# Kernel tuning notes

Measured on AMD Instinct MI355X. Metric: run time of the kernel, lower is better.

## Reference

```python
import jax, jax.numpy as jnp
import numpy as np


def setup_inputs() -> dict:
    key = jax.random.key(0)
    k1, k2, k3 = jax.random.split(key, 3)
    B, H, S, D = 1, 16, 2048, 64
    NPOS, HID = 64, 1024
    query = jax.random.normal(k1, (B, H, S, D), dtype=jnp.float32)
    attn_logits = jax.random.normal(k2, (B, H, S, S), dtype=jnp.float32)
    pos_emb = jax.random.normal(k3, (1, NPOS, HID), dtype=jnp.float32)
    return {"query": query, "attn_logits": attn_logits, "pos_emb": pos_emb}


def reference(query, attn_logits, pos_emb):
    # query: [B,H,S,D]; attn_logits: [B,H,S,S]; pos_emb: [1,NPOS,H*D]
    B, H, S, D = query.shape
    npos_max = pos_emb.shape[1]
    gates = jax.nn.sigmoid(attn_logits)
    # reverse cumsum along keys: position of each key relative to query
    pos = jnp.flip(jnp.cumsum(jnp.flip(gates, axis=-1), axis=-1), axis=-1)
    pos = jnp.minimum(pos, npos_max - 1)
    pos_ceil = jnp.ceil(pos).astype(jnp.int32)
    pos_floor = jnp.floor(pos).astype(jnp.int32)
    # split heads: [1,NPOS,H*D] -> [H,NPOS,D]
    pe = pos_emb.reshape(npos_max, H, D).transpose(1, 0, 2)
    # per-head position logits: [B,H,S,NPOS]
    logits_int = jnp.einsum('bhsd,hnd->bhsn', query, pe)
    logits_ceil = jnp.take_along_axis(logits_int, pos_ceil, axis=-1)
    logits_floor = jnp.take_along_axis(logits_int, pos_floor, axis=-1)
    w = pos - pos_floor  # fractional interpolation weight
    return logits_ceil * w + logits_floor * (1.0 - w)
```

## Files before the change

kernel.cpp:

```cpp
#include <hip/hip_runtime.h>

namespace {
constexpr int kH       = 16;
constexpr int kS       = 2048;
constexpr int kD       = 64;
constexpr int kNpos    = 64;
constexpr int kHid     = 1024;
constexpr int kChunk   = 256;
constexpr int kNChunks = kS / kChunk;
constexpr int kRowsPerBlock = 16;
}

__device__ __forceinline__ float dot4f(float4 a, float qx, float qy, float qz, float qw) {
    return fmaf(a.x, qx, fmaf(a.y, qy, fmaf(a.z, qz, a.w * qw)));
}

template <int CTRL, int ROWM>
__device__ __forceinline__ float dpp_add(float v) {
    int t = __builtin_amdgcn_update_dpp(0, __float_as_int(v), CTRL, ROWM, 0xf, true);
    return v + __int_as_float(t);
}

__device__ __forceinline__ float wave_incl_scan(float v) {
    v = dpp_add<0x111, 0xf>(v);
    v = dpp_add<0x112, 0xf>(v);
    v = dpp_add<0x114, 0xf>(v);
    v = dpp_add<0x118, 0xf>(v);
    v = dpp_add<0x142, 0xa>(v);
    v = dpp_add<0x143, 0xc>(v);
    return v;
}

__device__ __forceinline__ float bcast_lane(float v, int l) {
    return __int_as_float(__builtin_amdgcn_readlane(__float_as_int(v), l));
}

__device__ __forceinline__ void process_row(const float* __restrict__ arow,
                                            float* __restrict__ orow,
                                            float acc, float4 x0, int lane) {
    const float fill = bcast_lane(acc, kNpos - 1);
    float running = 0.0f;
    int c = kNChunks - 1;
    float4 x = x0;
    for (; c >= 0; --c) {
        if (c != kNChunks - 1)
            x = *reinterpret_cast<const float4*>(arow + c * kChunk + lane * 4);
        float g0 = 1.0f / (1.0f + __expf(-x.x));
        float g1 = 1.0f / (1.0f + __expf(-x.y));
        float g2 = 1.0f / (1.0f + __expf(-x.z));
        float g3 = 1.0f / (1.0f + __expf(-x.w));

        float e3 = g3;
        float e2 = e3 + g2;
        float e1 = e2 + g1;
        float e0 = e1 + g0;

        float incl  = wave_incl_scan(e0);
        float total = bcast_lane(incl, 63);
        float sfx   = running + (total - incl);

        float p[4] = {sfx + e0, sfx + e1, sfx + e2, sfx + e3};
        float r[4];
        #pragma unroll
        for (int i = 0; i < 4; ++i) {
            float pc = fminf(p[i], 63.0f);
            float fl = floorf(pc);
            float w  = pc - fl;
            int  fi  = (int)fl;
            int  ni  = (fi < kNpos - 1) ? fi + 1 : kNpos - 1;
            float lf = __shfl(acc, fi);
            float ln = __shfl(acc, ni);
            r[i] = fmaf(w, ln - lf, lf);
        }
        *reinterpret_cast<float4*>(orow + c * kChunk + lane * 4) =
            make_float4(r[0], r[1], r[2], r[3]);

        running += total;
        if (running >= 63.0f) break;
    }
    const int fillEnd = (c > 0) ? c * kChunk : 0;
    const float4 fv = make_float4(fill, fill, fill, fill);
    for (int j = lane * 4; j < fillEnd; j += 256) {
        *reinterpret_cast<float4*>(orow + j) = fv;
    }
}

__global__ __launch_bounds__(256) void cope_kernel(
    const float* __restrict__ query,
    const float* __restrict__ attn,
    const float* __restrict__ pos_emb,
    float* __restrict__ out)
{
    const int t    = threadIdx.x;
    const int lane = t & 63;
    const int wid  = t >> 6;
    const int row_base = blockIdx.x * kRowsPerBlock;
    const int h        = row_base >> 11;
    const int wrow = __builtin_amdgcn_readfirstlane(row_base + wid * 4);

    __shared__ float4 pe_lds[kNpos * 16];

    const float* arow = attn + (size_t)wrow * kS;
    float*       orow = out  + (size_t)wrow * kS;

    const int tail = (kNChunks - 1) * kChunk + lane * 4;
    float4 x0 = *reinterpret_cast<const float4*>(arow + 0 * kS + tail);
    float4 x1 = *reinterpret_cast<const float4*>(arow + 1 * kS + tail);
    float4 x2 = *reinterpret_cast<const float4*>(arow + 2 * kS + tail);
    float4 x3 = *reinterpret_cast<const float4*>(arow + 3 * kS + tail);

    #pragma unroll
    for (int k = 0; k < 4; ++k) {
        const int e = t + 256 * k;
        const int n = e >> 4;
        const int j = e & 15;
        float4 p = *reinterpret_cast<const float4*>(
            pos_emb + (size_t)n * kHid + h * kD + 4 * j);
        pe_lds[(n << 4) | (j ^ (n & 15))] = p;
    }
    __syncthreads();

    const float* qbase = query + (size_t)wrow * kD;
    float acc0 = 0.f, acc1 = 0.f, acc2 = 0.f, acc3 = 0.f;
    #pragma unroll 4
    for (int j = 0; j < 16; ++j) {
        float4 pe4 = pe_lds[(lane << 4) | (j ^ (lane & 15))];
        const float* q0 = qbase + 0 * kD + 4 * j;
        const float* q1 = qbase + 1 * kD + 4 * j;
        const float* q2 = qbase + 2 * kD + 4 * j;
        const float* q3 = qbase + 3 * kD + 4 * j;
        acc0 += dot4f(pe4, q0[0], q0[1], q0[2], q0[3]);
        acc1 += dot4f(pe4, q1[0], q1[1], q1[2], q1[3]);
        acc2 += dot4f(pe4, q2[0], q2[1], q2[2], q2[3]);
        acc3 += dot4f(pe4, q3[0], q3[1], q3[2], q3[3]);
    }

    process_row(arow + 0 * kS, orow + 0 * kS, acc0, x0, lane);
    process_row(arow + 1 * kS, orow + 1 * kS, acc1, x1, lane);
    process_row(arow + 2 * kS, orow + 2 * kS, acc2, x2, lane);
    process_row(arow + 3 * kS, orow + 3 * kS, acc3, x3, lane);
}

extern "C" void kernel_launch(void* const* d_in, const int* in_sizes, int n_in,
                              void* d_out, int out_size, void* d_ws, size_t ws_size,
                              hipStream_t stream) {
    const float* query   = (const float*)d_in[0];
    const float* attn    = (const float*)d_in[1];
    const float* pos_emb = (const float*)d_in[2];
    float* out = (float*)d_out;

    const int rows = kH * kS;
    dim3 grid(rows / kRowsPerBlock), block(256);
    cope_kernel<<<grid, block, 0, stream>>>(query, attn, pos_emb, out);
}
```

Before: 68.84 us.

## Split constant-fill stores into a separate streaming kernel before the tail kernel

Moves the constant fill of the leading output chunks into its own kernel. That kernel computes only the position-63 logit per row, using a wave reduction, and then issues unrolled float4 stores for the first seven chunks unconditionally. The second kernel does the sigmoid, suffix-scan and interpolation work from the row tail backwards and overwrites whatever part the early exit does not cover. The aim is to turn the bulk output writes into a simple store-only stream, free of the attention loads and scan dependencies. The cost is an extra launch, and any chunk the tail kernel processes is written twice.

```diff
diff --git a/kernel.cpp b/kernel.cpp
--- a/kernel.cpp
+++ b/kernel.cpp
@@ -9,6 +9,7 @@
 constexpr int kChunk   = 256;
 constexpr int kNChunks = kS / kChunk;
 constexpr int kRowsPerBlock = 16;
+constexpr int kFillChunks = kNChunks - 1;
 }
 
 __device__ __forceinline__ float dot4f(float4 a, float qx, float qy, float qz, float qw) {
@@ -35,14 +36,51 @@
     return __int_as_float(__builtin_amdgcn_readlane(__float_as_int(v), l));
 }
 
-__device__ __forceinline__ void process_row(const float* __restrict__ arow,
-                                            float* __restrict__ orow,
-                                            float acc, float4 x0, int lane) {
-    const float fill = bcast_lane(acc, kNpos - 1);
+__device__ __forceinline__ float wave_sum(float v) {
+    return bcast_lane(wave_incl_scan(v), 63);
+}
+
+__global__ __launch_bounds__(256) void cope_fill_kernel(
+    const float* __restrict__ query,
+    const float* __restrict__ pos_emb,
+    float* __restrict__ out)
+{
+    const int t    = threadIdx.x;
+    const int lane = t & 63;
+    const int wid  = t >> 6;
+    const int row_base = blockIdx.x * kRowsPerBlock;
+    const int h        = row_base >> 11;
+    const int wrow = __builtin_amdgcn_readfirstlane(row_base + wid * 4);
+
+    const float pe63 = pos_emb[(size_t)(kNpos - 1) * kHid + h * kD + lane];
+
+    const float* qrow = query + (size_t)wrow * kD;
+    const float f0 = wave_sum(qrow[0 * kD + lane] * pe63);
+    const float f1 = wave_sum(qrow[1 * kD + lane] * pe63);
+    const float f2 = wave_sum(qrow[2 * kD + lane] * pe63);
+    const float f3 = wave_sum(qrow[3 * kD + lane] * pe63);
+
+    float* orow = out + (size_t)wrow * kS;
+    const float4 v0 = make_float4(f0, f0, f0, f0);
+    const float4 v1 = make_float4(f1, f1, f1, f1);
+    const float4 v2 = make_float4(f2, f2, f2, f2);
+    const float4 v3 = make_float4(f3, f3, f3, f3);
+    #pragma unroll
+    for (int j = 0; j < kFillChunks; ++j) {
+        const int off = j * kChunk + lane * 4;
+        *reinterpret_cast<float4*>(orow + 0 * kS + off) = v0;
+        *reinterpret_cast<float4*>(orow + 1 * kS + off) = v1;
+        *reinterpret_cast<float4*>(orow + 2 * kS + off) = v2;
+        *reinterpret_cast<float4*>(orow + 3 * kS + off) = v3;
+    }
+}
+
+__device__ __forceinline__ void process_row_tail(const float* __restrict__ arow,
+                                                 float* __restrict__ orow,
+                                                 float acc, float4 x0, int lane) {
     float running = 0.0f;
-    int c = kNChunks - 1;
     float4 x = x0;
-    for (; c >= 0; --c) {
+    for (int c = kNChunks - 1; c >= 0; --c) {
         if (c != kNChunks - 1)
             x = *reinterpret_cast<const float4*>(arow + c * kChunk + lane * 4);
         float g0 = 1.0f / (1.0f + __expf(-x.x));
@@ -78,14 +116,9 @@
         running += total;
         if (running >= 63.0f) break;
     }
-    const int fillEnd = (c > 0) ? c * kChunk : 0;
-    const float4 fv = make_float4(fill, fill, fill, fill);
-    for (int j = lane * 4; j < fillEnd; j += 256) {
-        *reinterpret_cast<float4*>(orow + j) = fv;
-    }
 }
 
-__global__ __launch_bounds__(256) void cope_kernel(
+__global__ __launch_bounds__(256) void cope_tail_kernel(
     const float* __restrict__ query,
     const float* __restrict__ attn,
     const float* __restrict__ pos_emb,
@@ -135,10 +168,10 @@
         acc3 += dot4f(pe4, q3[0], q3[1], q3[2], q3[3]);
     }
 
-    process_row(arow + 0 * kS, orow + 0 * kS, acc0, x0, lane);
-    process_row(arow + 1 * kS, orow + 1 * kS, acc1, x1, lane);
-    process_row(arow + 2 * kS, orow + 2 * kS, acc2, x2, lane);
-    process_row(arow + 3 * kS, orow + 3 * kS, acc3, x3, lane);
+    process_row_tail(arow + 0 * kS, orow + 0 * kS, acc0, x0, lane);
+    process_row_tail(arow + 1 * kS, orow + 1 * kS, acc1, x1, lane);
+    process_row_tail(arow + 2 * kS, orow + 2 * kS, acc2, x2, lane);
+    process_row_tail(arow + 3 * kS, orow + 3 * kS, acc3, x3, lane);
 }
 
 extern "C" void kernel_launch(void* const* d_in, const int* in_sizes, int n_in,
@@ -151,5 +184,7 @@
 
     const int rows = kH * kS;
     dim3 grid(rows / kRowsPerBlock), block(256);
-    cope_kernel<<<grid, block, 0, stream>>>(query, attn, pos_emb, out);
+
+    cope_fill_kernel<<<grid, block, 0, stream>>>(query, pos_emb, out);
+    cope_tail_kernel<<<grid, block, 0, stream>>>(query, attn, pos_emb, out);
 }
```

Result: slower. 72.11 us (+4.8%).
